# Kernel tuning notes

Hardware: AMD Instinct MI355X
Metric: run time of the kernel (lower is better)

Reference implementation:

```python
import jax, jax.numpy as jnp
import numpy as np

B, T, HID = 2, 2048, 2048
N_HEADS, N_KV, HEAD_DIM = 32, 8, 64
THETA = 10000.0
SCALE = HEAD_DIM ** -0.5
STEPS = 2  # entries already in cache before this call (step_idx)


def _rope_cos_sin(pos):
    # pos: [B, T] int -> cos/sin [B, T, HEAD_DIM]
    inv_freq = 1.0 / (THETA ** (jnp.arange(0, HEAD_DIM, 2, dtype=jnp.float32) / HEAD_DIM))
    freqs = pos.astype(jnp.float32)[..., None] * inv_freq  # [B,T,D/2]
    emb = jnp.concatenate([freqs, freqs], axis=-1)
    return jnp.cos(emb), jnp.sin(emb)


def _rotate_half(x):
    x1, x2 = jnp.split(x, 2, axis=-1)
    return jnp.concatenate([-x2, x1], axis=-1)


def setup_inputs() -> dict:
    key = jax.random.key(0)
    ks = jax.random.split(key, 8)
    combined_states = jax.random.normal(ks[0], (B, T, 2 * HID), dtype=jnp.float32)
    # additive causal mask: 0 on/below diagonal, large negative above
    causal = jnp.tril(jnp.ones((T, T), dtype=bool))
    attention_mask = jnp.where(causal, 0.0, -1e9).astype(jnp.float32)[None, None].repeat(B, axis=0)
    position_ids = jnp.broadcast_to(jnp.arange(T, dtype=jnp.int32), (B, T))
    prev_k = jax.random.normal(ks[1], (STEPS, B, N_HEADS, T, HEAD_DIM), dtype=jnp.float32)
    prev_v = jax.random.normal(ks[2], (STEPS, B, N_HEADS, T, HEAD_DIM), dtype=jnp.float32)
    Wq = 0.02 * jax.random.normal(ks[3], (2 * HID, N_HEADS * HEAD_DIM), dtype=jnp.float32)
    Wk = 0.02 * jax.random.normal(ks[4], (2 * HID, N_KV * HEAD_DIM), dtype=jnp.float32)
    Wv = 0.02 * jax.random.normal(ks[5], (2 * HID, N_KV * HEAD_DIM), dtype=jnp.float32)
    Wo = 0.02 * jax.random.normal(ks[6], (N_HEADS * HEAD_DIM, HID), dtype=jnp.float32)
    return {"combined_states": combined_states, "attention_mask": attention_mask,
            "position_ids": position_ids, "prev_k": prev_k, "prev_v": prev_v,
            "Wq": Wq, "Wk": Wk, "Wv": Wv, "Wo": Wo}


def reference(combined_states, attention_mask, position_ids, prev_k, prev_v, Wq, Wk, Wv, Wo):
    b, t, _ = combined_states.shape
    step_idx = prev_k.shape[0]  # len(cache_k) before append
    groups = N_HEADS // N_KV

    # fused QKV projection -> [B, H, T, D]
    q = (combined_states @ Wq).reshape(b, t, N_HEADS, HEAD_DIM).transpose(0, 2, 1, 3)
    k = (combined_states @ Wk).reshape(b, t, N_KV, HEAD_DIM).transpose(0, 2, 1, 3)
    v = (combined_states @ Wv).reshape(b, t, N_KV, HEAD_DIM).transpose(0, 2, 1, 3)

    # RoPE with phase shift by step_idx
    cos, sin = _rope_cos_sin(position_ids + step_idx)
    cos, sin = cos[:, None], sin[:, None]  # [B,1,T,D]
    q = q * cos + _rotate_half(q) * sin
    k = k * cos + _rotate_half(k) * sin

    # GQA expansion (repeat_interleave over head dim)
    k = jnp.repeat(k, groups, axis=1)
    v = jnp.repeat(v, groups, axis=1)

    # cache after append: [prev_0, prev_1, ..., k_new]; k0 = cache[0], later = cache[1:]
    k0, v0 = prev_k[0], prev_v[0]
    later_k = jnp.concatenate([prev_k[1:], k[None]], axis=0)  # [S, B, H, T, D], S = step_idx
    later_v = jnp.concatenate([prev_v[1:], v[None]], axis=0)

    # block attention over K_0 plus growing diagonal terms
    attn = jnp.einsum('bhtd,bhsd->bhts', q, k0) * SCALE + attention_mask  # [B,H,T,T]
    diag = jnp.einsum('bhtd,sbhtd->bhts', q, later_k) * SCALE             # [B,H,T,S]
    logits = jnp.concatenate([attn, diag], axis=-1)                        # [B,H,T,T+S]
    probs = jax.nn.softmax(logits.astype(jnp.float32), axis=-1).astype(q.dtype)

    out = jnp.einsum('bhts,bhsd->bhtd', probs[..., :t], v0)
    out = out + jnp.einsum('bhts,sbhtd->bhtd', probs[..., t:], later_v)
    out = out.transpose(0, 2, 1, 3).reshape(b, t, N_HEADS * HEAD_DIM)
    return out @ Wo
```

## Files before the change

kernel.cpp:

```cpp
#include <hip/hip_runtime.h>

#define B_    2
#define T_    2048
#define HID_  2048
#define NH_   32
#define NKV_  8
#define HD_   64
#define STEPS_ 2
#define SCALE_ 0.125f
#define CSC_  0.18033688011112042f

typedef float   f32x4  __attribute__((ext_vector_type(4)));
typedef __bf16  bf16x8 __attribute__((ext_vector_type(8)));
typedef unsigned short u16x8 __attribute__((ext_vector_type(8)));

__device__ __forceinline__ unsigned short f2bf(float f) {
  unsigned int u = __builtin_bit_cast(unsigned int, f);
  u = (u + 0x7fffu + ((u >> 16) & 1u)) >> 16;
  return (unsigned short)u;
}
__device__ __forceinline__ float bf2f(unsigned short h) {
  unsigned int u = ((unsigned int)h) << 16;
  return __builtin_bit_cast(float, u);
}
__device__ __forceinline__ bf16x8 frag_ld(const unsigned short* p) {
  u16x8 v = *(const u16x8*)p;
  return __builtin_bit_cast(bf16x8, v);
}
__device__ __forceinline__ f32x4 mfma16(bf16x8 a, bf16x8 b, f32x4 c) {
  return __builtin_amdgcn_mfma_f32_16x16x32_bf16(a, b, c, 0, 0, 0);
}
__device__ __forceinline__ void async_cp16(const void* g, void* l) {
  __builtin_amdgcn_global_load_lds(
      (const __attribute__((address_space(1))) void*)g,
      (__attribute__((address_space(3))) void*)l, 16, 0, 0);
}
__device__ __forceinline__ unsigned int cvtpk_bf16(float lo, float hi) {
  unsigned int r;
  asm("v_cvt_pk_bf16_f32 %0, %1, %2" : "=v"(r) : "v"(lo), "v"(hi));
  return r;
}

__global__ __launch_bounds__(256) void convert_bf16(const float* __restrict__ in,
                                                    unsigned short* __restrict__ out,
                                                    int n4) {
  int idx = blockIdx.x * 256 + threadIdx.x;
  if (idx < n4) {
    float4 v = ((const float4*)in)[idx];
    ushort4 o;
    o.x = f2bf(v.x); o.y = f2bf(v.y); o.z = f2bf(v.z); o.w = f2bf(v.w);
    ((ushort4*)out)[idx] = o;
  }
}

__global__ __launch_bounds__(256) void transpose_f32_bf16_ld(const float* __restrict__ in,
                                                             unsigned short* __restrict__ out,
                                                             int K, int N, int ldo) {
  __shared__ float tile[64][65];
  int n0 = blockIdx.x * 64, k0 = blockIdx.y * 64;
  int c = threadIdx.x & 63, w = threadIdx.x >> 6;
#pragma unroll
  for (int i = 0; i < 16; i++) {
    int r = w * 16 + i;
    tile[r][c] = in[(size_t)(k0 + r) * N + n0 + c];
  }
  __syncthreads();
#pragma unroll
  for (int i = 0; i < 16; i++) {
    int rr = w * 16 + i;
    out[(size_t)(n0 + rr) * ldo + k0 + c] = f2bf(tile[c][rr]);
  }
}

__global__ __launch_bounds__(256) void transpose_v0(const float* __restrict__ v0,
                                                    unsigned short* __restrict__ v0t) {
  __shared__ float tile[64][65];
  int s0 = blockIdx.x * 64;
  int bh = blockIdx.y;
  const float* src = v0 + (size_t)bh * T_ * HD_;
  unsigned short* dst = v0t + (size_t)bh * HD_ * T_;
  int c = threadIdx.x & 63, w = threadIdx.x >> 6;
#pragma unroll
  for (int i = 0; i < 16; i++) {
    int r = w * 16 + i;
    tile[r][c] = src[(size_t)(s0 + r) * HD_ + c];
  }
  __syncthreads();
#pragma unroll
  for (int i = 0; i < 16; i++) {
    int rr = w * 16 + i;
    dst[(size_t)rr * T_ + s0 + c] = f2bf(tile[c][rr]);
  }
}

#define SBAR  do { __builtin_amdgcn_sched_barrier(0); __builtin_amdgcn_s_barrier(); \
                   __builtin_amdgcn_sched_barrier(0); } while (0)
#define LGKM0 do { asm volatile("s_waitcnt lgkmcnt(0)" ::: "memory"); \
                   __builtin_amdgcn_sched_barrier(0); } while (0)
#define VM2   do { asm volatile("s_waitcnt vmcnt(2)" ::: "memory"); } while (0)
#define VM0   do { asm volatile("s_waitcnt vmcnt(0)" ::: "memory"); } while (0)

template <int NF>
__global__ __launch_bounds__(512, 2) void gemm128_bt(const unsigned short* __restrict__ A,
                                                     const unsigned short* __restrict__ Bt,
                                                     float* __restrict__ C,
                                                     int M, int N, int K) {
  constexpr int NHF = NF / 2;
  constexpr int BROWS = 128 + NF * 64;
  __shared__ __attribute__((aligned(128))) unsigned short smem[2][BROWS * 64];

  const int tid  = threadIdx.x;
  const int lane = tid & 63;
  const int wid  = tid >> 6;
  const int wr   = wid >> 2;
  const int wc   = wid & 3;
  const int la   = lane & 15;
  const int lq   = lane >> 4;
  const int sw   = la & 7;
  const int m0   = blockIdx.x * 128;
  const int n0   = blockIdx.y * (NF * 64);

  const int sr = lane >> 3;
  const int sl = (lane & 7) ^ sr;

  const unsigned short* gA[2];
  const unsigned short* gB[NHF][2];
#pragma unroll
  for (int is = 0; is < 2; ++is) {
    int r = (wid * 2 + is) * 8 + sr;
    gA[is] = A + (size_t)(m0 + r) * K + sl * 8;
#pragma unroll
    for (int u = 0; u < NHF; ++u)
      gB[u][is] = Bt + (size_t)(n0 + u * 128 + r) * K + sl * 8;
  }

#define G_STG_A(buf, kt) do { \
    async_cp16(gA[0] + (size_t)(kt) * 64, &smem[buf][(wid * 2 + 0) * 512]); \
    async_cp16(gA[1] + (size_t)(kt) * 64, &smem[buf][(wid * 2 + 1) * 512]); \
  } while (0)
#define G_STG_B(buf, u, kt) do { \
    async_cp16(gB[u][0] + (size_t)(kt) * 64, &smem[buf][(128 + (u) * 128) * 64 + (wid * 2 + 0) * 512]); \
    async_cp16(gB[u][1] + (size_t)(kt) * 64, &smem[buf][(128 + (u) * 128) * 64 + (wid * 2 + 1) * 512]); \
  } while (0)

  f32x4  acc[4][NF] = {};
  bf16x8 aR[2][2], b0r[NHF][2], b1r[NHF][2];

#define G_RD_A(buf, qm) do { \
    const unsigned short* rp_ = &smem[buf][0]; \
    _Pragma("unroll") \
    for (int i_ = 0; i_ < 2; ++i_) { \
      int ro_ = (wr * 64 + (qm) * 32 + i_ * 16 + la) * 64; \
      aR[i_][0] = frag_ld(rp_ + ro_ + (((0 + lq) ^ sw) << 3)); \
      aR[i_][1] = frag_ld(rp_ + ro_ + (((4 + lq) ^ sw) << 3)); \
    } \
  } while (0)
#define G_RD_B(buf, qn, breg) do { \
    const unsigned short* rp_ = &smem[buf][128 * 64]; \
    _Pragma("unroll") \
    for (int j_ = 0; j_ < NHF; ++j_) { \
      int ro_ = (wc * (NF * 16) + (qn) * (NF * 8) + j_ * 16 + la) * 64; \
      breg[j_][0] = frag_ld(rp_ + ro_ + (((0 + lq) ^ sw) << 3)); \
      breg[j_][1] = frag_ld(rp_ + ro_ + (((4 + lq) ^ sw) << 3)); \
    } \
  } while (0)
#define G_MMA(qm, qn, breg) do { \
    _Pragma("unroll") \
    for (int i_ = 0; i_ < 2; ++i_) \
      _Pragma("unroll") \
      for (int j_ = 0; j_ < NHF; ++j_) { \
        f32x4 c_ = acc[(qm) * 2 + i_][(qn) * NHF + j_]; \
        c_ = mfma16(aR[i_][0], breg[j_][0], c_); \
        c_ = mfma16(aR[i_][1], breg[j_][1], c_); \
        acc[(qm) * 2 + i_][(qn) * NHF + j_] = c_; \
      } \
  } while (0)

  G_STG_A(0, 0);
#pragma unroll
  for (int u = 0; u < NHF; ++u) G_STG_B(0, u, 0);
  if constexpr (NF == 6) G_STG_B(1, 2, 1); else G_STG_A(1, 1);
  VM2;
  SBAR;

  const int NI = K >> 7;
  for (int it = 0; it < NI; ++it) {
    const int e = it * 2;
    const bool pf = (it + 1 < NI);
    G_RD_A(0, 0);
    G_RD_B(0, 0, b0r);
    if constexpr (NF == 6) G_STG_A(1, e + 1); else G_STG_B(1, 0, e + 1);
    SBAR; LGKM0;
    __builtin_amdgcn_s_setprio(1); G_MMA(0, 0, b0r); __builtin_amdgcn_s_setprio(0);
    SBAR;
    G_RD_B(0, 1, b1r);
    if constexpr (NF == 6) G_STG_B(1, 0, e + 1); else G_STG_B(1, 1, e + 1);
    SBAR; LGKM0;
    __builtin_amdgcn_s_setprio(1); G_MMA(0, 1, b1r); __builtin_amdgcn_s_setprio(0);
    SBAR;
    G_RD_A(0, 1);
    if constexpr (NF == 6) G_STG_B(1, 1, e + 1);
    SBAR; LGKM0;
    __builtin_amdgcn_s_setprio(1); G_MMA(1, 1, b1r); __builtin_amdgcn_s_setprio(0);
    SBAR;
    if (pf) G_STG_A(0, e + 2);
    SBAR; LGKM0;
    __builtin_amdgcn_s_setprio(1); G_MMA(1, 0, b0r); __builtin_amdgcn_s_setprio(0);
    if (pf) { VM2; } else { VM0; }
    SBAR;
    G_RD_A(1, 0);
    G_RD_B(1, 0, b0r);
    if (pf) G_STG_B(0, 0, e + 2);
    SBAR; LGKM0;
    __builtin_amdgcn_s_setprio(1); G_MMA(0, 0, b0r); __builtin_amdgcn_s_setprio(0);
    SBAR;
    G_RD_B(1, 1, b1r);
    if (pf) G_STG_B(0, 1, e + 2);
    SBAR; LGKM0;
    __builtin_amdgcn_s_setprio(1); G_MMA(0, 1, b1r); __builtin_amdgcn_s_setprio(0);
    SBAR;
    G_RD_A(1, 1);
    if constexpr (NF == 6) { if (pf) G_STG_B(0, 2, e + 2); }
    SBAR; LGKM0;
    __builtin_amdgcn_s_setprio(1); G_MMA(1, 1, b1r); __builtin_amdgcn_s_setprio(0);
    SBAR;
    if constexpr (NF == 6) { if (pf) G_STG_B(1, 2, e + 3); }
    else                   { if (pf) G_STG_A(1, e + 3); }
    SBAR; LGKM0;
    __builtin_amdgcn_s_setprio(1); G_MMA(1, 0, b0r); __builtin_amdgcn_s_setprio(0);
    VM2;
    SBAR;
  }

#pragma unroll
  for (int mf = 0; mf < 4; ++mf) {
    int row = m0 + wr * 64 + mf * 16 + lq * 4;
#pragma unroll
    for (int nf = 0; nf < NF; ++nf) {
      int col = n0 + wc * (NF * 16) + nf * 16 + la;
#pragma unroll
      for (int r = 0; r < 4; ++r)
        C[(size_t)(row + r) * N + col] = acc[mf][nf][r];
    }
  }
#undef G_STG_A
#undef G_STG_B
#undef G_RD_A
#undef G_RD_B
#undef G_MMA
}

__global__ __launch_bounds__(256) void rope_kernel(const float* __restrict__ QKV,
                                                   const int* __restrict__ pos_ids,
                                                   unsigned short* __restrict__ q_b,
                                                   float* __restrict__ knew) {
  int idx = blockIdx.x * 256 + threadIdx.x;
  const int total = B_ * T_ * (NH_ + NKV_) * 32;
  if (idx >= total) return;
  int i = idx & 31;
  int tmp = idx >> 5;
  int hh = tmp % (NH_ + NKV_);
  int bt = tmp / (NH_ + NKV_);
  int t = bt & (T_ - 1);
  int b = bt >> 11;
  int pos = pos_ids[bt] + STEPS_;
  float inv = exp2f(-(float)i * (13.287712379549449f / 32.0f));
  float ang = (float)pos * inv;
  float sn, cs;
  sincosf(ang, &sn, &cs);
  const float* rowp = QKV + (size_t)bt * 3072;
  if (hh < NH_) {
    float x1 = rowp[hh * 64 + i];
    float x2 = rowp[hh * 64 + 32 + i];
    float y1 = (x1 * cs - x2 * sn) * CSC_;
    float y2 = (x2 * cs + x1 * sn) * CSC_;
    size_t o = ((size_t)(b * NH_ + hh) * T_ + t) * HD_ + i;
    q_b[o] = f2bf(y1);
    q_b[o + 32] = f2bf(y2);
  } else {
    int kv = hh - NH_;
    float x1 = rowp[2048 + kv * 64 + i];
    float x2 = rowp[2048 + kv * 64 + 32 + i];
    float y1 = x1 * cs - x2 * sn;
    float y2 = x2 * cs + x1 * sn;
    size_t o = ((size_t)(b * NKV_ + kv) * T_ + t) * HD_ + i;
    knew[o] = y1;
    knew[o + 32] = y2;
  }
}

__global__ __launch_bounds__(256, 3) void flash_kernel(const unsigned short* __restrict__ qb,
                                                       const unsigned short* __restrict__ k0b,
                                                       const unsigned short* __restrict__ v0t,
                                                       const float* __restrict__ prev_k,
                                                       const float* __restrict__ prev_v,
                                                       const float* __restrict__ knew,
                                                       const float* __restrict__ QKV,
                                                       unsigned short* __restrict__ attnout) {
  __shared__ unsigned short sK[2][64 * 64];
  __shared__ unsigned short sV[2][64 * 64];
  __shared__ unsigned short sP[4][2][16 * 72];

  const int tid = threadIdx.x;
  const int lane = tid & 63;
  const int wave = tid >> 6;
  const int la = lane & 15;
  const int lq = lane >> 4;
  const int swz = la & 7;

  const int id = blockIdx.x;
  const int bh = (id & 7) * 8 + ((id >> 3) & 7);
  const int qt = 15 - (id >> 6);

  const size_t bhs = (size_t)bh;
  const unsigned short* gK = k0b + bhs * T_ * HD_;
  const unsigned short* gV = v0t + bhs * HD_ * T_;

  const int rb0 = qt * 128 + wave * 32;
  const int ktd = rb0 >> 6;
  const int ktmax = 2 * qt + 1;

  bf16x8 aq[2][2];
#pragma unroll
  for (int f = 0; f < 2; f++) {
    const unsigned short* qp = qb + (bhs * T_ + rb0 + f * 16 + la) * HD_;
    aq[f][0] = frag_ld(qp + lq * 8);
    aq[f][1] = frag_ld(qp + 32 + lq * 8);
  }

  f32x4 o[2][4] = {};
  float m_f[2] = {-1e30f, -1e30f};
  float l_p[2] = {0.0f, 0.0f};

  const int lrow = lane >> 3;
  const int lcb = (lane & 7) ^ lrow;

  {
    unsigned short* kd = &sK[0][wave * 1024];
    unsigned short* vd = &sV[0][wave * 1024];
    async_cp16(gK + (size_t)(wave * 16 + lrow) * HD_ + lcb * 8, kd);
    async_cp16(gK + (size_t)(wave * 16 + 8 + lrow) * HD_ + lcb * 8, kd + 512);
    async_cp16(gV + (size_t)(wave * 16 + lrow) * T_ + lcb * 8, vd);
    async_cp16(gV + (size_t)(wave * 16 + 8 + lrow) * T_ + lcb * 8, vd + 512);
  }
  __syncthreads();

  int cur = 0;
  for (int kt = 0; kt <= ktmax; ++kt) {
    if (kt < ktmax) {
      const int nk = (kt + 1) * 64;
      unsigned short* kd = &sK[cur ^ 1][wave * 1024];
      unsigned short* vd = &sV[cur ^ 1][wave * 1024];
      async_cp16(gK + (size_t)(nk + wave * 16 + lrow) * HD_ + lcb * 8, kd);
      async_cp16(gK + (size_t)(nk + wave * 16 + 8 + lrow) * HD_ + lcb * 8, kd + 512);
      async_cp16(gV + (size_t)(wave * 16 + lrow) * T_ + nk + lcb * 8, vd);
      async_cp16(gV + (size_t)(wave * 16 + 8 + lrow) * T_ + nk + lcb * 8, vd + 512);
    }

    if (kt <= ktd) {
      const unsigned short* kb = &sK[cur][0];
      const unsigned short* vb = &sV[cur][0];

      bf16x8 bk0[4], bk1[4];
#pragma unroll
      for (int nb = 0; nb < 4; nb++) {
        const unsigned short* rp = kb + (nb * 16 + la) * 64;
        bk0[nb] = frag_ld(rp + ((lq ^ swz) << 3));
        bk1[nb] = frag_ld(rp + (((lq + 4) ^ swz) << 3));
      }
      f32x4 s[2][4];
      __builtin_amdgcn_s_setprio(1);
#pragma unroll
      for (int f = 0; f < 2; f++)
#pragma unroll
        for (int nb = 0; nb < 4; nb++) {
          f32x4 z = {0.f, 0.f, 0.f, 0.f};
          z = mfma16(bk0[nb], aq[f][0], z);
          z = mfma16(bk1[nb], aq[f][1], z);
          s[f][nb] = z;
        }
      __builtin_amdgcn_s_setprio(0);

      bf16x8 bv0[4], bv1[4];
#pragma unroll
      for (int jd = 0; jd < 4; jd++) {
        const unsigned short* rp = vb + (jd * 16 + la) * 64;
        bv0[jd] = frag_ld(rp + ((lq ^ swz) << 3));
        bv1[jd] = frag_ld(rp + (((lq + 4) ^ swz) << 3));
      }

      const bool diag = (kt == ktd);
#pragma unroll
      for (int f = 0; f < 2; f++) {
        const int qrow = rb0 + f * 16 + la;
        if (diag) {
#pragma unroll
          for (int nb = 0; nb < 4; nb++)
#pragma unroll
            for (int r = 0; r < 4; r++) {
              int key = kt * 64 + nb * 16 + lq * 4 + r;
              s[f][nb][r] = (key <= qrow) ? s[f][nb][r] : -1e30f;
            }
        }
        float t0 = fmaxf(fmaxf(s[f][0][0], s[f][0][1]), fmaxf(s[f][0][2], s[f][0][3]));
        float t1 = fmaxf(fmaxf(s[f][1][0], s[f][1][1]), fmaxf(s[f][1][2], s[f][1][3]));
        float t2 = fmaxf(fmaxf(s[f][2][0], s[f][2][1]), fmaxf(s[f][2][2], s[f][2][3]));
        float t3 = fmaxf(fmaxf(s[f][3][0], s[f][3][1]), fmaxf(s[f][3][2], s[f][3][3]));
        float tm = fmaxf(fmaxf(t0, t1), fmaxf(t2, t3));
        const bool resc = __any(tm > m_f[f] + 8.0f);
        if (resc) {
          tm = fmaxf(tm, __shfl_xor(tm, 16));
          tm = fmaxf(tm, __shfl_xor(tm, 32));
          float mn = fmaxf(m_f[f], tm);
          float al = exp2f(m_f[f] - mn);
          m_f[f] = mn;
          l_p[f] *= al;
          float a0 = __shfl(al, lq * 4 + 0);
          float a1 = __shfl(al, lq * 4 + 1);
          float a2 = __shfl(al, lq * 4 + 2);
          float a3 = __shfl(al, lq * 4 + 3);
#pragma unroll
          for (int jd = 0; jd < 4; jd++) {
            o[f][jd][0] *= a0;
            o[f][jd][1] *= a1;
            o[f][jd][2] *= a2;
            o[f][jd][3] *= a3;
          }
        }
        float ls = 0.0f;
#pragma unroll
        for (int nb = 0; nb < 4; nb++)
#pragma unroll
          for (int r = 0; r < 4; r++) {
            float p = exp2f(s[f][nb][r] - m_f[f]);
            s[f][nb][r] = p;
            ls += p;
          }
        l_p[f] += ls;
        unsigned short* pw = &sP[wave][f][0];
#pragma unroll
        for (int nb = 0; nb < 4; nb++) {
          unsigned int p01 = cvtpk_bf16(s[f][nb][0], s[f][nb][1]);
          unsigned int p23 = cvtpk_bf16(s[f][nb][2], s[f][nb][3]);
          unsigned long long pq = ((unsigned long long)p23 << 32) | (unsigned long long)p01;
          *(unsigned long long*)(pw + la * 72 + nb * 16 + lq * 4) = pq;
        }
      }

#pragma unroll
      for (int f = 0; f < 2; f++) {
        const unsigned short* pr = &sP[wave][f][0];
        bf16x8 ap0 = frag_ld(&pr[la * 72 + lq * 8]);
        bf16x8 ap1 = frag_ld(&pr[la * 72 + 32 + lq * 8]);
        __builtin_amdgcn_s_setprio(1);
#pragma unroll
        for (int jd = 0; jd < 4; jd++) {
          o[f][jd] = mfma16(ap0, bv0[jd], o[f][jd]);
          o[f][jd] = mfma16(ap1, bv1[jd], o[f][jd]);
        }
        __builtin_amdgcn_s_setprio(0);
      }
    }
    __syncthreads();
    cur ^= 1;
  }

#pragma unroll
  for (int f = 0; f < 2; f++) {
    l_p[f] += __shfl_xor(l_p[f], 16);
    l_p[f] += __shfl_xor(l_p[f], 32);
  }

  const int bI = bh >> 5;
  const int hI = bh & 31;
  const int kvI = hI >> 2;
  const size_t P1 = (size_t)B_ * NH_ * T_ * HD_;
  const float* k1base = prev_k + P1 + bhs * T_ * HD_;
  const float* v1base = prev_v + P1 + bhs * T_ * HD_;
  const float* knbase = knew + ((size_t)bI * NKV_ + kvI) * T_ * HD_;
  const float* vnbase = QKV + (size_t)bI * T_ * 3072 + 2560 + kvI * 64;
  unsigned short* aobase = attnout + (size_t)bI * T_ * (NH_ * HD_) + hI * HD_;

#pragma unroll
  for (int f = 0; f < 2; f++) {
    const int rowA = rb0 + f * 16 + la;
    const float* k1p = k1base + (size_t)rowA * HD_;
    const float* knp = knbase + (size_t)rowA * HD_;
    float e1 = 0.f, e2 = 0.f;
#pragma unroll
    for (int h2 = 0; h2 < 2; h2++) {
      const int dd = h2 * 32 + lq * 8;
#pragma unroll
      for (int j = 0; j < 8; j++) {
        float qv = (float)aq[f][h2][j];
        e1 = fmaf(qv, k1p[dd + j], e1);
        e2 = fmaf(qv, knp[dd + j], e2);
      }
    }
    e1 += __shfl_xor(e1, 16); e1 += __shfl_xor(e1, 32);
    e2 += __shfl_xor(e2, 16); e2 += __shfl_xor(e2, 32);
    float mx = fmaxf(m_f[f], fmaxf(e1, e2));
    float w0 = exp2f(m_f[f] - mx);
    float w1 = exp2f(e1 - mx);
    float w2 = exp2f(e2 - mx);
    float inv = 1.0f / (l_p[f] * w0 + w1 + w2);
    float s0 = w0 * inv, s1 = w1 * inv, s2 = w2 * inv;
    float a0[4], a1[4], a2[4];
#pragma unroll
    for (int r = 0; r < 4; r++) {
      a0[r] = __shfl(s0, lq * 4 + r);
      a1[r] = __shfl(s1, lq * 4 + r);
      a2[r] = __shfl(s2, lq * 4 + r);
    }
#pragma unroll
    for (int r = 0; r < 4; r++) {
      const int rowO = rb0 + f * 16 + lq * 4 + r;
      const float* v1p = v1base + (size_t)rowO * HD_;
      const float* vnp = vnbase + (size_t)rowO * 3072;
      unsigned short* aop = aobase + (size_t)rowO * (NH_ * HD_);
#pragma unroll
      for (int jd = 0; jd < 4; jd++) {
        int d = jd * 16 + la;
        float out = o[f][jd][r] * a0[r] + v1p[d] * a1[r] + vnp[d] * a2[r];
        aop[d] = f2bf(out);
      }
    }
  }
}

#define OFF_QKV   ((size_t)0)
#define OFF_XB    ((size_t)50331648)
#define OFF_WQKVT ((size_t)83886080)
#define OFF_WOT   ((size_t)109051904)
#define OFF_QB    ((size_t)117440512)
#define OFF_K0B   ((size_t)134217728)
#define OFF_V0T   ((size_t)150994944)
#define OFF_KNEW  ((size_t)167772160)
#define OFF_ML    ((size_t)176160768)

extern "C" void kernel_launch(void* const* d_in, const int* in_sizes, int n_in,
                              void* d_out, int out_size, void* d_ws, size_t ws_size,
                              hipStream_t stream) {
  const float* X = (const float*)d_in[0];
  const int* pos = (const int*)d_in[2];
  const float* prevk = (const float*)d_in[3];
  const float* prevv = (const float*)d_in[4];
  const float* Wq = (const float*)d_in[5];
  const float* Wk = (const float*)d_in[6];
  const float* Wv = (const float*)d_in[7];
  const float* Wo = (const float*)d_in[8];

  char* ws = (char*)d_ws;
  float* QKV = (float*)(ws + OFF_QKV);
  unsigned short* Xb = (unsigned short*)(ws + OFF_XB);
  unsigned short* WqkvT = (unsigned short*)(ws + OFF_WQKVT);
  unsigned short* attnout = (unsigned short*)(ws + OFF_WQKVT);
  unsigned short* WoT = (unsigned short*)(ws + OFF_WOT);
  unsigned short* q_b = (unsigned short*)(ws + OFF_QB);
  unsigned short* k0b = (unsigned short*)(ws + OFF_K0B);
  unsigned short* v0t = (unsigned short*)(ws + OFF_V0T);
  float* knew = (float*)(ws + OFF_KNEW);

  convert_bf16<<<16384, 256, 0, stream>>>(X, Xb, 4194304);
  transpose_f32_bf16_ld<<<dim3(32, 64), 256, 0, stream>>>(Wq, WqkvT, 4096, 2048, 4096);
  transpose_f32_bf16_ld<<<dim3(8, 64), 256, 0, stream>>>(Wk, WqkvT + (size_t)2048 * 4096, 4096, 512, 4096);
  transpose_f32_bf16_ld<<<dim3(8, 64), 256, 0, stream>>>(Wv, WqkvT + (size_t)2560 * 4096, 4096, 512, 4096);
  transpose_f32_bf16_ld<<<dim3(32, 32), 256, 0, stream>>>(Wo, WoT, 2048, 2048, 2048);
  convert_bf16<<<8192, 256, 0, stream>>>(prevk, k0b, 2097152);
  transpose_v0<<<dim3(32, 64), 256, 0, stream>>>(prevv, v0t);

  gemm128_bt<6><<<dim3(32, 8), 512, 0, stream>>>(Xb, WqkvT, QKV, 4096, 3072, 4096);

  rope_kernel<<<20480, 256, 0, stream>>>(QKV, pos, q_b, knew);

  flash_kernel<<<1024, 256, 0, stream>>>(q_b, k0b, v0t, prevk, prevv, knew, QKV, attnout);

  gemm128_bt<4><<<dim3(32, 8), 512, 0, stream>>>(attnout, WoT, (float*)d_out, 4096, 2048, 2048);
}
```

Measured before the change: 503.1 us.

## Merge QKV weight transposes, remap GEMM tiles, shrink flash P buffer for occupancy

The three Wq/Wk/Wv transpose launches become one kernel that picks its source by block index, saving two launches. The GEMM block index is permuted so blocks running together share A/B tiles and reuse L2 better. In the flash kernel the per-wave P staging buffer is cut to a single swizzled 16x64 tile reused for both fragments, and the V fragment loads move after the softmax. Together with launch bounds going from 3 to 4 blocks per CU, this aims at higher occupancy but risks register spills.

```diff
diff --git a/kernel.cpp b/kernel.cpp
--- a/kernel.cpp
+++ b/kernel.cpp
@@ -53,6 +53,31 @@
   }
 }
 
+__global__ __launch_bounds__(256) void transpose_wqkv(const float* __restrict__ Wq,
+                                                      const float* __restrict__ Wk,
+                                                      const float* __restrict__ Wv,
+                                                      unsigned short* __restrict__ out) {
+  __shared__ float tile[64][65];
+  int bx = blockIdx.x;
+  const float* in; int N; int nbase;
+  if (bx < 32)      { in = Wq; N = 2048; nbase = 0;    }
+  else if (bx < 40) { in = Wk; N = 512;  nbase = 2048; bx -= 32; }
+  else              { in = Wv; N = 512;  nbase = 2560; bx -= 40; }
+  int n0 = bx * 64, k0 = blockIdx.y * 64;
+  int c = threadIdx.x & 63, w = threadIdx.x >> 6;
+#pragma unroll
+  for (int i = 0; i < 16; i++) {
+    int r = w * 16 + i;
+    tile[r][c] = in[(size_t)(k0 + r) * N + n0 + c];
+  }
+  __syncthreads();
+#pragma unroll
+  for (int i = 0; i < 16; i++) {
+    int rr = w * 16 + i;
+    out[(size_t)(nbase + n0 + rr) * 4096 + k0 + c] = f2bf(tile[c][rr]);
+  }
+}
+
 __global__ __launch_bounds__(256) void transpose_f32_bf16_ld(const float* __restrict__ in,
                                                              unsigned short* __restrict__ out,
                                                              int K, int N, int ldo) {
@@ -117,8 +142,11 @@
   const int la   = lane & 15;
   const int lq   = lane >> 4;
   const int sw   = la & 7;
-  const int m0   = blockIdx.x * 128;
-  const int n0   = blockIdx.y * (NF * 64);
+
+  const int lid = blockIdx.x + blockIdx.y * 32;
+  const int nl  = (lid & 7) * 32 + (lid >> 3);
+  const int m0  = (nl & 31) * 128;
+  const int n0  = (nl >> 5) * (NF * 64);
 
   const int sr = lane >> 3;
   const int sl = (lane & 7) ^ sr;
@@ -289,7 +317,7 @@
   }
 }
 
-__global__ __launch_bounds__(256, 3) void flash_kernel(const unsigned short* __restrict__ qb,
+__global__ __launch_bounds__(256, 4) void flash_kernel(const unsigned short* __restrict__ qb,
                                                        const unsigned short* __restrict__ k0b,
                                                        const unsigned short* __restrict__ v0t,
                                                        const float* __restrict__ prev_k,
@@ -299,7 +327,7 @@
                                                        unsigned short* __restrict__ attnout) {
   __shared__ unsigned short sK[2][64 * 64];
   __shared__ unsigned short sV[2][64 * 64];
-  __shared__ unsigned short sP[4][2][16 * 72];
+  __shared__ unsigned short sP[4][16 * 64];
 
   const int tid = threadIdx.x;
   const int lane = tid & 63;
@@ -307,6 +335,7 @@
   const int la = lane & 15;
   const int lq = lane >> 4;
   const int swz = la & 7;
+  const int swp = la & 6;
 
   const int id = blockIdx.x;
   const int bh = (id & 7) * 8 + ((id >> 3) & 7);
@@ -380,14 +409,6 @@
           s[f][nb] = z;
         }
       __builtin_amdgcn_s_setprio(0);
-
-      bf16x8 bv0[4], bv1[4];
-#pragma unroll
-      for (int jd = 0; jd < 4; jd++) {
-        const unsigned short* rp = vb + (jd * 16 + la) * 64;
-        bv0[jd] = frag_ld(rp + ((lq ^ swz) << 3));
-        bv1[jd] = frag_ld(rp + (((lq + 4) ^ swz) << 3));
-      }
 
       const bool diag = (kt == ktd);
 #pragma unroll
@@ -437,21 +458,28 @@
             ls += p;
           }
         l_p[f] += ls;
-        unsigned short* pw = &sP[wave][f][0];
+      }
+
+      bf16x8 bv0[4], bv1[4];
+#pragma unroll
+      for (int jd = 0; jd < 4; jd++) {
+        const unsigned short* rp = vb + (jd * 16 + la) * 64;
+        bv0[jd] = frag_ld(rp + ((lq ^ swz) << 3));
+        bv1[jd] = frag_ld(rp + (((lq + 4) ^ swz) << 3));
+      }
+
+      unsigned short* pw = &sP[wave][0];
+#pragma unroll
+      for (int f = 0; f < 2; f++) {
 #pragma unroll
         for (int nb = 0; nb < 4; nb++) {
           unsigned int p01 = cvtpk_bf16(s[f][nb][0], s[f][nb][1]);
           unsigned int p23 = cvtpk_bf16(s[f][nb][2], s[f][nb][3]);
           unsigned long long pq = ((unsigned long long)p23 << 32) | (unsigned long long)p01;
-          *(unsigned long long*)(pw + la * 72 + nb * 16 + lq * 4) = pq;
+          *(unsigned long long*)(pw + la * 64 + (((nb * 4 + lq) ^ swp) << 2)) = pq;
         }
-      }
-
-#pragma unroll
-      for (int f = 0; f < 2; f++) {
-        const unsigned short* pr = &sP[wave][f][0];
-        bf16x8 ap0 = frag_ld(&pr[la * 72 + lq * 8]);
-        bf16x8 ap1 = frag_ld(&pr[la * 72 + 32 + lq * 8]);
+        bf16x8 ap0 = frag_ld(&pw[la * 64 + (((lq * 2) ^ swp) << 2)]);
+        bf16x8 ap1 = frag_ld(&pw[la * 64 + ((8 + ((lq * 2) ^ swp)) << 2)]);
         __builtin_amdgcn_s_setprio(1);
 #pragma unroll
         for (int jd = 0; jd < 4; jd++) {
@@ -562,9 +590,7 @@
   float* knew = (float*)(ws + OFF_KNEW);
 
   convert_bf16<<<16384, 256, 0, stream>>>(X, Xb, 4194304);
-  transpose_f32_bf16_ld<<<dim3(32, 64), 256, 0, stream>>>(Wq, WqkvT, 4096, 2048, 4096);
-  transpose_f32_bf16_ld<<<dim3(8, 64), 256, 0, stream>>>(Wk, WqkvT + (size_t)2048 * 4096, 4096, 512, 4096);
-  transpose_f32_bf16_ld<<<dim3(8, 64), 256, 0, stream>>>(Wv, WqkvT + (size_t)2560 * 4096, 4096, 512, 4096);
+  transpose_wqkv<<<dim3(48, 64), 256, 0, stream>>>(Wq, Wk, Wv, WqkvT);
   transpose_f32_bf16_ld<<<dim3(32, 32), 256, 0, stream>>>(Wo, WoT, 2048, 2048, 2048);
   convert_bf16<<<8192, 256, 0, stream>>>(prevk, k0b, 2097152);
   transpose_v0<<<dim3(32, 64), 256, 0, stream>>>(prevv, v0t);
```

After: 526.3 us. 1.05x slower.
